# Kernel tuning notes

Measured on AMD Instinct MI355X. Metric: run time of the kernel, lower is better.

The kernel has to match this reference:

```python
import jax, jax.numpy as jnp
import numpy as np

LN2 = 0.6931471805599453

def ssp(x):
    # 'shifted_sp' activation: softplus(x) - log(2)
    return jax.nn.softplus(x) - LN2

def _res_chain(x, W1, b1, W2, b2):
    # PhysNetResidual chain: x <- lin2(ssp(lin1(ssp(x)))) + x
    # W1/W2: [n_res, F, F], b1/b2: [n_res, F]
    for j in range(W1.shape[0]):
        h = ssp(x) @ W1[j] + b1[j]
        x = ssp(h) @ W2[j] + b2[j] + x
    return x

def _physnet_module(feat, radial_aev, idx12, p):
    (W_I, b_I, W_J, b_J, W_gate, gvec, W_int, b_int,
     ri_W1, ri_b1, ri_W2, ri_b2,
     ra_W1, ra_b1, ra_W2, ra_b2,
     ro_W1, ro_b1, ro_W2, ro_b2, W_out, b_out) = p
    N, F = feat.shape
    # self term (no species are dummy -> non_dummy indexing is identity)
    h_self = ssp(ssp(feat) @ W_I + b_I)                       # [N,F]
    # pair messages
    gate = radial_aev @ W_gate                                 # [P,F] (no bias)
    f12 = feat[idx12]                                          # [2,P,F] gather
    fm = ssp(ssp(f12) @ W_J + b_J)                             # [2,P,F]
    pair_msg = gate[None] * fm                                 # [2,P,F]
    proto = jnp.zeros_like(feat).at[idx12.reshape(-1)].add(
        pair_msg.reshape(-1, F))                               # scatter-add
    proto = proto + h_self
    msg = _res_chain(proto, ri_W1, ri_b1, ri_W2, ri_b2)
    feat2 = feat * gvec + ssp(msg) @ W_int + b_int
    feat2 = _res_chain(feat2, ra_W1, ra_b1, ra_W2, ra_b2)
    e = ssp(_res_chain(feat2, ro_W1, ro_b1, ro_W2, ro_b2)) @ W_out + b_out  # [N]
    return e, feat2

def setup_inputs() -> dict:
    key = jax.random.key(0)
    L, F, R = 5, 128, 64
    M, A = 128, 64
    N = M * A
    P = 400000
    ks = jax.random.split(key, 20)
    s = 0.05  # small weight scale keeps activations stable across 5 modules
    inp = {
        'species': jax.random.randint(ks[0], (M, A), 0, 4, dtype=jnp.int32),
        'features': jax.random.normal(ks[1], (N, F), jnp.float32),
        'radial_aev': jax.random.uniform(ks[2], (P, R), jnp.float32),
        'atom_index12': jax.random.randint(ks[3], (2, P), 0, N, dtype=jnp.int32),
        'W_I': jax.random.normal(ks[4], (L, F, F)) * s,
        'b_I': jnp.zeros((L, F)),
        'W_J': jax.random.normal(ks[5], (L, F, F)) * s,
        'b_J': jnp.zeros((L, F)),
        'W_gate': jax.random.normal(ks[6], (L, R, F)) * s,
        'gvec': jnp.ones((L, F)),
        'W_int': jax.random.normal(ks[7], (L, F, F)) * s,
        'b_int': jnp.zeros((L, F)),
        'ri_W1': jax.random.normal(ks[8], (L, 3, F, F)) * s,
        'ri_b1': jnp.zeros((L, 3, F)),
        'ri_W2': jax.random.normal(ks[9], (L, 3, F, F)) * s,
        'ri_b2': jnp.zeros((L, 3, F)),
        'ra_W1': jax.random.normal(ks[10], (L, 2, F, F)) * s,
        'ra_b1': jnp.zeros((L, 2, F)),
        'ra_W2': jax.random.normal(ks[11], (L, 2, F, F)) * s,
        'ra_b2': jnp.zeros((L, 2, F)),
        'ro_W1': jax.random.normal(ks[12], (L, 1, F, F)) * s,
        'ro_b1': jnp.zeros((L, 1, F)),
        'ro_W2': jax.random.normal(ks[13], (L, 1, F, F)) * s,
        'ro_b2': jnp.zeros((L, 1, F)),
        'W_out': jax.random.normal(ks[14], (L, F)) * s,
        'b_out': jnp.zeros((L,)),
    }
    return inp

def reference(species, features, radial_aev, atom_index12,
              W_I, b_I, W_J, b_J, W_gate, gvec, W_int, b_int,
              ri_W1, ri_b1, ri_W2, ri_b2,
              ra_W1, ra_b1, ra_W2, ra_b2,
              ro_W1, ro_b1, ro_W2, ro_b2, W_out, b_out):
    M, A = species.shape
    params = (W_I, b_I, W_J, b_J, W_gate, gvec, W_int, b_int,
              ri_W1, ri_b1, ri_W2, ri_b2,
              ra_W1, ra_b1, ra_W2, ra_b2,
              ro_W1, ro_b1, ro_W2, ro_b2, W_out, b_out)
    feat = features
    energies = jnp.zeros((M * A,), features.dtype)
    for l in range(W_I.shape[0]):  # fixed small module loop
        p = tuple(arr[l] for arr in params)
        e, feat = _physnet_module(feat, radial_aev, atom_index12, p)
        energies = energies + e
    return energies.reshape(M, A), feat
```

## Files before the change

### kernel.cpp

```cpp
#include <hip/hip_runtime.h>


#define LN2F 0.69314718055994530942f
#define NB 128

using short8  = __attribute__((ext_vector_type(8))) short;
using float4v = __attribute__((ext_vector_type(4))) float;
typedef const __attribute__((address_space(1))) unsigned int* gas1_t;
typedef __attribute__((address_space(3))) unsigned int* las3_t;

__device__ __forceinline__ float sspf(float x) {
  float ax = fabsf(x);
  return fmaxf(x, 0.0f) + __logf(1.0f + __expf(-ax)) - LN2F;
}

__device__ __forceinline__ unsigned short f2bf(float x) {
  return (unsigned short)((__float_as_uint(x) + 0x8000u) >> 16);
}

__device__ __forceinline__ unsigned short f2bf_ne(float x) {
  unsigned int u = __float_as_uint(x);
  u += 0x7fffu + ((u >> 16) & 1u);
  return (unsigned short)(u >> 16);
}

__device__ __forceinline__ void dma16(const void* g, void* l) {
  __builtin_amdgcn_global_load_lds((gas1_t)(unsigned long long)g,
                                   (las3_t)(unsigned long long)l, 16, 0, 0);
}

__device__ __forceinline__ void dma32k(const unsigned short* g, unsigned short* l,
                                       int w, int lane) {
  const char* gb = (const char*)g + w * 2048 + lane * 16;
  char* lb = (char*)l + w * 2048;
  dma16(gb, lb);
  dma16(gb + 1024, lb + 1024);
}
__device__ __forceinline__ void dma16k(const unsigned short* g, unsigned short* l,
                                       int w, int lane) {
  dma16((const char*)g + w * 1024 + lane * 16, (char*)l + w * 1024);
}

__global__ __launch_bounds__(256) void hist_pass(const int* __restrict__ idx,
                                                 unsigned int* __restrict__ H,
                                                 int n2p, int C) {
  __shared__ unsigned int h[8192];
  int b = blockIdx.x, tid = threadIdx.x;
  for (int i = tid; i < 8192; i += 256) h[i] = 0;
  __syncthreads();
  int s = b * C, e = min(s + C, n2p);
  for (int i = s + tid; i < e; i += 256) atomicAdd(&h[idx[i]], 1u);
  __syncthreads();
  for (int i = tid; i < 8192; i += 256) H[(size_t)b * 8192 + i] = h[i];
}

__global__ __launch_bounds__(256) void col_scan(unsigned int* __restrict__ H,
                                                unsigned int* __restrict__ tot) {
  int a = blockIdx.x * 256 + threadIdx.x;
  unsigned int run = 0;
  for (int b = 0; b < NB; ++b) {
    unsigned int v = H[(size_t)b * 8192 + a];
    H[(size_t)b * 8192 + a] = run;
    run += v;
  }
  tot[a] = run;
}

__global__ __launch_bounds__(256) void scan_kernel(const unsigned int* __restrict__ cnt,
                                                   unsigned int* __restrict__ off, int NA) {
  int t = threadIdx.x;
  unsigned int local[32], s = 0;
#pragma unroll
  for (int i = 0; i < 32; ++i) { local[i] = cnt[t * 32 + i]; s += local[i]; }
  unsigned int v = s;
  int lane = t & 63, w = t >> 6;
#pragma unroll
  for (int o = 1; o < 64; o <<= 1) {
    unsigned int u = __shfl_up(v, o, 64);
    if (lane >= o) v += u;
  }
  __shared__ unsigned int wt4[4];
  if (lane == 63) wt4[w] = v;
  __syncthreads();
  unsigned int base = 0;
  for (int k = 0; k < w; ++k) base += wt4[k];
  unsigned int excl = base + v - s;
#pragma unroll
  for (int i = 0; i < 32; ++i) { off[t * 32 + i] = excl; excl += local[i]; }
  if (t == 255) off[NA] = excl;
}

__global__ __launch_bounds__(256) void place_pass(const int* __restrict__ idx,
                                                  const unsigned int* __restrict__ H,
                                                  const unsigned int* __restrict__ off,
                                                  unsigned int* __restrict__ pairid,
                                                  int P, int C) {
  __shared__ unsigned int pos[8192];
  int b = blockIdx.x, tid = threadIdx.x;
  for (int i = tid; i < 8192; i += 256)
    pos[i] = off[i] + H[(size_t)b * 8192 + i];
  __syncthreads();
  int n2p = 2 * P;
  int s = b * C, e = min(s + C, n2p);
  for (int i = s + tid; i < e; i += 256) {
    int a = idx[i];
    unsigned int p = atomicAdd(&pos[a], 1u);
    pairid[p] = (i >= P) ? (unsigned int)(i - P) : (unsigned int)i;
  }
}

__global__ __launch_bounds__(256) void gather_kernel(const float* __restrict__ radial,
                                                     const unsigned int* __restrict__ off,
                                                     const unsigned int* __restrict__ pairid,
                                                     float* __restrict__ S) {
  __shared__ float red[3][64];
  int a = blockIdx.x;
  int lane = threadIdx.x & 63, w = threadIdx.x >> 6;
  unsigned int b = off[a], e = off[a + 1];
  float acc = 0.0f;
  for (unsigned int base = b + w; base < e; base += 32) {
    unsigned int pp[8];
    float vv[8];
#pragma unroll
    for (int k = 0; k < 8; ++k) {
      unsigned int j = base + 4 * k;
      pp[k] = pairid[j < e ? j : b];
    }
#pragma unroll
    for (int k = 0; k < 8; ++k) vv[k] = radial[(size_t)pp[k] * 64 + lane];
#pragma unroll
    for (int k = 0; k < 8; ++k) {
      unsigned int j = base + 4 * k;
      acc += (j < e) ? vv[k] : 0.0f;
    }
  }
  if (w > 0) red[w - 1][lane] = acc;
  __syncthreads();
  if (w == 0) {
    acc += red[0][lane] + red[1][lane] + red[2][lane];
    S[(size_t)a * 64 + lane] = acc;
  }
}

struct PrepArgs {
  const float* src[80];
  int isgate[80];
};

__global__ __launch_bounds__(256) void prep_weights(PrepArgs A, unsigned short* __restrict__ Wt) {
  int m = blockIdx.x;
  const float* s = A.src[m];
  unsigned short* d = Wt + (size_t)m * 16384;
  if (!A.isgate[m]) {
    for (int it = 0; it < 8; ++it) {
      int q = threadIdx.x + it * 256;
      int n = q & 127, j = q >> 7;
      unsigned short tmp[8];
#pragma unroll
      for (int cc = 0; cc < 8; ++cc) tmp[cc] = f2bf_ne(s[(8 * j + cc) * 128 + n]);
      *(uint4*)(d + (n * 16 + (j ^ (n & 15))) * 8) = *(uint4*)tmp;
    }
  } else {
    for (int it = 0; it < 4; ++it) {
      int q = threadIdx.x + it * 256;
      int n = q & 127, j = q >> 7;
      unsigned short tmp[8];
#pragma unroll
      for (int cc = 0; cc < 8; ++cc) tmp[cc] = f2bf_ne(s[(8 * j + cc) * 128 + n]);
      *(uint4*)(d + (n * 8 + (j ^ (n & 7))) * 8) = *(uint4*)tmp;
    }
  }
}

struct BiasArgs {
  const float* p[17];
  int stride[17];
  const float* b_out;
};

__global__ __launch_bounds__(256) void pack_bias(BiasArgs B, float* __restrict__ dst) {
  int l = blockIdx.x;
  for (int i = threadIdx.x; i < 17 * 128; i += 256) {
    int s = i >> 7;
    dst[(size_t)l * 2304 + i] = B.p[s][l * B.stride[s] + (i & 127)];
  }
  if (threadIdx.x == 0) dst[(size_t)l * 2304 + 17 * 128] = B.b_out[l];
}

struct ChainArgs {
  const float* feat_in;
  const float* S;
  const unsigned short* wt;
  const float* bias_pack;
  float* feat_out;
  float* energy;
};

__device__ __forceinline__ void gemm128s(const unsigned short* sA_, const unsigned short* sW,
                                         int arow, int col0, int l16, int quad, float4v* acc) {
  const unsigned short* ar = sA_ + (arow + l16) * 136 + quad * 8;
  short8 a0 = *(const short8*)(ar);
  short8 a1 = *(const short8*)(ar + 32);
  short8 a2 = *(const short8*)(ar + 64);
  short8 a3 = *(const short8*)(ar + 96);
  const unsigned short* bb = sW + col0 * 128;
  *acc = __builtin_amdgcn_mfma_f32_16x16x32_bf16(a0, *(const short8*)(bb + ((quad + 0) ^ l16) * 8), *acc, 0, 0, 0);
  *acc = __builtin_amdgcn_mfma_f32_16x16x32_bf16(a1, *(const short8*)(bb + ((quad + 4) ^ l16) * 8), *acc, 0, 0, 0);
  *acc = __builtin_amdgcn_mfma_f32_16x16x32_bf16(a2, *(const short8*)(bb + ((quad + 8) ^ l16) * 8), *acc, 0, 0, 0);
  *acc = __builtin_amdgcn_mfma_f32_16x16x32_bf16(a3, *(const short8*)(bb + ((quad + 12) ^ l16) * 8), *acc, 0, 0, 0);
}

__device__ __forceinline__ void gemm64s(const unsigned short* sS_, const unsigned short* sW,
                                        int arow, int col0, int l16, int quad, float4v* acc) {
  const unsigned short* ar = sS_ + (arow + l16) * 72 + quad * 8;
  short8 a0 = *(const short8*)(ar);
  short8 a1 = *(const short8*)(ar + 32);
  int l8 = l16 & 7;
  const unsigned short* bb = sW + col0 * 64;
  *acc = __builtin_amdgcn_mfma_f32_16x16x32_bf16(a0, *(const short8*)(bb + ((quad + 0) ^ l8) * 8), *acc, 0, 0, 0);
  *acc = __builtin_amdgcn_mfma_f32_16x16x32_bf16(a1, *(const short8*)(bb + ((quad + 4) ^ l8) * 8), *acc, 0, 0, 0);
}

__device__ __forceinline__ void write_ssp_A(unsigned short* sA_, const float4v v,
                                            int arow, int col0, int quad) {
#pragma unroll
  for (int r = 0; r < 4; ++r)
    sA_[(arow + quad * 4 + r) * 136 + col0] = f2bf(sspf(v[r]));
}

__global__ __launch_bounds__(1024, 4) void chain_kernel(ChainArgs A) {
  __shared__ __align__(16) unsigned short swb[2][16384];
  __shared__ __align__(16) unsigned short sA[2][32 * 136];
  __shared__ __align__(16) unsigned short sS[32 * 72];
  __shared__ float sBias[2304];
  __shared__ float sE[32];

  const int tid  = threadIdx.x;
  const int row0 = blockIdx.x * 32;
  const int lane = tid & 63;
  const int w    = tid >> 6;
  const int g    = w >> 3;
  const int c    = w & 7;
  const int l16  = lane & 15;
  const int quad = lane >> 4;
  const int arow = 16 * g;
  const int col0 = 16 * c + l16;

  dma16k(A.wt, swb[0], w, lane);

  for (int i = tid; i < 32 * 64; i += 1024) {
    int r = i >> 6, k = i & 63;
    sS[r * 72 + k] = f2bf(A.S[(size_t)(row0 + r) * 64 + k]);
  }
  for (int i = tid; i < 32 * 128; i += 1024) {
    int r = i >> 7, k = i & 127;
    sA[0][r * 136 + k] = f2bf(sspf(A.feat_in[(size_t)(row0 + r) * 128 + k]));
  }
  float4v ff;
#pragma unroll
  for (int r = 0; r < 4; ++r)
    ff[r] = A.feat_in[(size_t)(row0 + arow + quad * 4 + r) * 128 + col0];
  if (tid < 32) sE[tid] = 0.0f;
  __syncthreads();

  const float4v Z = {0.f, 0.f, 0.f, 0.f};
  float4v gG, fm, xf, t4;
  float p0 = 0.f, p1 = 0.f, p2 = 0.f, p3 = 0.f, bsum = 0.f;

#pragma unroll 1
  for (int l = 0; l < 5; ++l) {
    const size_t slot0 = (size_t)l * 16 * 16384;

    dma32k(A.wt + slot0 + 16384, swb[1], w, lane);
    for (int i = tid; i < 2304; i += 1024) sBias[i] = A.bias_pack[(size_t)l * 2304 + i];
    gG = Z;
    gemm64s(sS, swb[0], arow, col0, l16, quad, &gG);
    __syncthreads();

    dma32k(A.wt + slot0 + 2 * 16384, swb[0], w, lane);
    fm = Z;
    gemm128s(sA[0], swb[1], arow, col0, l16, quad, &fm);
    {
      float bv = sBias[0 * 128 + col0];
#pragma unroll
      for (int r = 0; r < 4; ++r) fm[r] = sspf(fm[r] + bv);
    }
    __syncthreads();

    dma32k(A.wt + slot0 + 3 * 16384, swb[1], w, lane);
    t4 = Z;
    gemm128s(sA[0], swb[0], arow, col0, l16, quad, &t4);
    {
      float bv = sBias[1 * 128 + col0];
#pragma unroll
      for (int r = 0; r < 4; ++r) xf[r] = fm[r] * gG[r] + sspf(t4[r] + bv);
    }
    write_ssp_A(sA[1], xf, arow, col0, quad);
    __syncthreads();

#pragma unroll
    for (int jj = 0; jj < 3; ++jj) {
      const int th = 3 + 2 * jj;
      dma32k(A.wt + slot0 + (size_t)(th + 1) * 16384, swb[th & 1 ? 0 : 1], w, lane);
      t4 = Z;
      gemm128s(sA[1], swb[th & 1], arow, col0, l16, quad, &t4);
      {
        float bv = sBias[(th - 1) * 128 + col0];
#pragma unroll
        for (int r = 0; r < 4; ++r) t4[r] += bv;
      }
      write_ssp_A(sA[0], t4, arow, col0, quad);
      __syncthreads();

      const int tx = th + 1;
      dma32k(A.wt + slot0 + (size_t)(tx + 1) * 16384, swb[tx & 1 ? 0 : 1], w, lane);
      t4 = Z;
      gemm128s(sA[0], swb[tx & 1], arow, col0, l16, quad, &t4);
      {
        float bv = sBias[(tx - 1) * 128 + col0];
#pragma unroll
        for (int r = 0; r < 4; ++r) xf[r] += t4[r] + bv;
      }
      write_ssp_A(sA[1], xf, arow, col0, quad);
      __syncthreads();
    }

    dma32k(A.wt + slot0 + 10 * 16384, swb[0], w, lane);
    t4 = Z;
    gemm128s(sA[1], swb[1], arow, col0, l16, quad, &t4);
    {
      float bv = sBias[8 * 128 + col0];
      float gv = sBias[15 * 128 + col0];
#pragma unroll
      for (int r = 0; r < 4; ++r) xf[r] = ff[r] * gv + t4[r] + bv;
    }
    write_ssp_A(sA[0], xf, arow, col0, quad);
    __syncthreads();

#pragma unroll
    for (int jj = 0; jj < 2; ++jj) {
      const int th = 10 + 2 * jj;
      dma32k(A.wt + slot0 + (size_t)(th + 1) * 16384, swb[th & 1 ? 0 : 1], w, lane);
      t4 = Z;
      gemm128s(sA[0], swb[th & 1], arow, col0, l16, quad, &t4);
      {
        float bv = sBias[(th - 1) * 128 + col0];
#pragma unroll
        for (int r = 0; r < 4; ++r) t4[r] += bv;
      }
      write_ssp_A(sA[1], t4, arow, col0, quad);
      __syncthreads();

      const int tx = th + 1;
      dma32k(A.wt + slot0 + (size_t)(tx + 1) * 16384, swb[tx & 1 ? 0 : 1], w, lane);
      t4 = Z;
      gemm128s(sA[1], swb[tx & 1], arow, col0, l16, quad, &t4);
      {
        float bv = sBias[(tx - 1) * 128 + col0];
#pragma unroll
        for (int r = 0; r < 4; ++r) xf[r] += t4[r] + bv;
      }
      write_ssp_A(sA[0], xf, arow, col0, quad);
      __syncthreads();
    }

    ff = xf;
    if (l == 4) {
#pragma unroll
      for (int r = 0; r < 4; ++r)
        A.feat_out[(size_t)(row0 + arow + quad * 4 + r) * 128 + col0] = xf[r];
    }

    dma32k(A.wt + slot0 + 15 * 16384, swb[1], w, lane);
    t4 = Z;
    gemm128s(sA[0], swb[0], arow, col0, l16, quad, &t4);
    {
      float bv = sBias[13 * 128 + col0];
#pragma unroll
      for (int r = 0; r < 4; ++r) t4[r] += bv;
    }
    write_ssp_A(sA[1], t4, arow, col0, quad);
    __syncthreads();

    if (l < 4) dma16k(A.wt + slot0 + 16 * 16384, swb[0], w, lane);
    t4 = Z;
    gemm128s(sA[1], swb[1], arow, col0, l16, quad, &t4);
    {
      float bv = sBias[14 * 128 + col0];
      float wv = sBias[16 * 128 + col0];
      p0 += sspf(xf[0] + t4[0] + bv) * wv;
      p1 += sspf(xf[1] + t4[1] + bv) * wv;
      p2 += sspf(xf[2] + t4[2] + bv) * wv;
      p3 += sspf(xf[3] + t4[3] + bv) * wv;
    }
    bsum += sBias[17 * 128];
    __syncthreads();
  }

#pragma unroll
  for (int o = 1; o < 16; o <<= 1) {
    p0 += __shfl_xor(p0, o, 64);
    p1 += __shfl_xor(p1, o, 64);
    p2 += __shfl_xor(p2, o, 64);
    p3 += __shfl_xor(p3, o, 64);
  }
  if (l16 == 0) {
    atomicAdd(&sE[arow + quad * 4 + 0], p0);
    atomicAdd(&sE[arow + quad * 4 + 1], p1);
    atomicAdd(&sE[arow + quad * 4 + 2], p2);
    atomicAdd(&sE[arow + quad * 4 + 3], p3);
  }
  __syncthreads();
  if (tid < 32) A.energy[row0 + tid] = sE[tid] + bsum;
}

extern "C" void kernel_launch(void* const* d_in, const int* in_sizes, int n_in,
                              void* d_out, int out_size, void* d_ws, size_t ws_size,
                              hipStream_t stream) {
  const float* features = (const float*)d_in[1];
  const float* radial   = (const float*)d_in[2];
  const int*   idx12    = (const int*)  d_in[3];
  const float* W_I    = (const float*)d_in[4];
  const float* b_I    = (const float*)d_in[5];
  const float* W_J    = (const float*)d_in[6];
  const float* b_J    = (const float*)d_in[7];
  const float* W_gate = (const float*)d_in[8];
  const float* gvec   = (const float*)d_in[9];
  const float* W_int  = (const float*)d_in[10];
  const float* b_int  = (const float*)d_in[11];
  const float* ri_W1  = (const float*)d_in[12];
  const float* ri_b1  = (const float*)d_in[13];
  const float* ri_W2  = (const float*)d_in[14];
  const float* ri_b2  = (const float*)d_in[15];
  const float* ra_W1  = (const float*)d_in[16];
  const float* ra_b1  = (const float*)d_in[17];
  const float* ra_W2  = (const float*)d_in[18];
  const float* ra_b2  = (const float*)d_in[19];
  const float* ro_W1  = (const float*)d_in[20];
  const float* ro_b1  = (const float*)d_in[21];
  const float* ro_W2  = (const float*)d_in[22];
  const float* ro_b2  = (const float*)d_in[23];
  const float* W_out  = (const float*)d_in[24];
  const float* b_out  = (const float*)d_in[25];

  const int N = in_sizes[1] / 128;
  const int P = in_sizes[3] / 2;
  const int L = in_sizes[25];
  const int n2p = 2 * P;
  const int C = (n2p + NB - 1) / NB;

  float* S = (float*)d_ws;
  float* bias_pack = S + (size_t)N * 64;
  unsigned short* Wt = (unsigned short*)(bias_pack + 5 * 2304);
  unsigned int* H      = (unsigned int*)(Wt + (size_t)80 * 16384);
  unsigned int* tot    = H + (size_t)NB * 8192;
  unsigned int* off    = tot + N;
  unsigned int* pairid = off + N + 4;

  PrepArgs pa;
  for (int l = 0; l < L; ++l) {
    const float* fx[16] = {
      W_gate + l * 8192,
      W_J + l * 16384, W_I + l * 16384,
      ri_W1 + (l * 3 + 0) * 16384, ri_W2 + (l * 3 + 0) * 16384,
      ri_W1 + (l * 3 + 1) * 16384, ri_W2 + (l * 3 + 1) * 16384,
      ri_W1 + (l * 3 + 2) * 16384, ri_W2 + (l * 3 + 2) * 16384,
      W_int + l * 16384,
      ra_W1 + (l * 2 + 0) * 16384, ra_W2 + (l * 2 + 0) * 16384,
      ra_W1 + (l * 2 + 1) * 16384, ra_W2 + (l * 2 + 1) * 16384,
      ro_W1 + l * 16384, ro_W2 + l * 16384 };
    for (int t = 0; t < 16; ++t) { pa.src[l * 16 + t] = fx[t]; pa.isgate[l * 16 + t] = (t == 0); }
  }
  prep_weights<<<80, 256, 0, stream>>>(pa, Wt);

  BiasArgs ba;
  const float* bp[17] = { b_J, b_I,
    ri_b1, ri_b2, ri_b1 + 128, ri_b2 + 128, ri_b1 + 256, ri_b2 + 256,
    b_int, ra_b1, ra_b2, ra_b1 + 128, ra_b2 + 128, ro_b1, ro_b2, gvec, W_out };
  int st[17] = {128,128, 384,384,384,384,384,384, 128, 256,256,256,256, 128,128,128,128};
  for (int q = 0; q < 17; ++q) { ba.p[q] = bp[q]; ba.stride[q] = st[q]; }
  ba.b_out = b_out;
  pack_bias<<<5, 256, 0, stream>>>(ba, bias_pack);

  hist_pass<<<NB, 256, 0, stream>>>(idx12, H, n2p, C);
  col_scan<<<32, 256, 0, stream>>>(H, tot);
  scan_kernel<<<1, 256, 0, stream>>>(tot, off, N);
  place_pass<<<NB, 256, 0, stream>>>(idx12, H, off, pairid, P, C);
  gather_kernel<<<N, 256, 0, stream>>>(radial, off, pairid, S);

  ChainArgs ca;
  ca.feat_in   = features;
  ca.S         = S;
  ca.wt        = Wt;
  ca.bias_pack = bias_pack;
  ca.energy    = (float*)d_out;
  ca.feat_out  = (float*)d_out + N;
  chain_kernel<<<N / 32, 1024, 0, stream>>>(ca);
}
```

Before: 347.3 us.

## Merge prep kernels, fold scan into place pass, vectorize gather, restructure chain pipeline

Combines weight prep, bias packing and histogram into one launch, and folds the global scan into each place_pass block so the single-block scan launch disappears. The gather now loads float4 rows, with 16 lanes per pair, and reduces with shuffles. The chain kernel keeps the gate weight in its own LDS buffer, double-buffers the bias pack and prefetches the next module's weights and bias. It also precomputes per-lane LDS pointers through macros. The aim is fewer kernel launches, less serialization between module iterations, and cheaper address arithmetic, paid for with more LDS per block and redundant scan work in every place_pass block.

```diff
diff --git a/kernel.cpp b/kernel.cpp
--- a/kernel.cpp
+++ b/kernel.cpp
@@ -41,17 +41,60 @@
   dma16((const char*)g + w * 1024 + lane * 16, (char*)l + w * 1024);
 }
 
-__global__ __launch_bounds__(256) void hist_pass(const int* __restrict__ idx,
-                                                 unsigned int* __restrict__ H,
-                                                 int n2p, int C) {
+struct K1Args {
+  const float* wsrc[80];
+  int isgate[80];
+  const float* bp[17];
+  int bstride[17];
+  const float* b_out;
+  const int* idx;
+  unsigned short* Wt;
+  float* bias_pack;
+  unsigned int* H;
+  int n2p, C;
+};
+
+__global__ __launch_bounds__(256) void k1_prep(K1Args K) {
   __shared__ unsigned int h[8192];
   int b = blockIdx.x, tid = threadIdx.x;
-  for (int i = tid; i < 8192; i += 256) h[i] = 0;
-  __syncthreads();
-  int s = b * C, e = min(s + C, n2p);
-  for (int i = s + tid; i < e; i += 256) atomicAdd(&h[idx[i]], 1u);
-  __syncthreads();
-  for (int i = tid; i < 8192; i += 256) H[(size_t)b * 8192 + i] = h[i];
+  if (b < 80) {
+    const float* s = K.wsrc[b];
+    unsigned short* d = K.Wt + (size_t)b * 16384;
+    if (!K.isgate[b]) {
+      for (int it = 0; it < 8; ++it) {
+        int q = tid + it * 256;
+        int n = q & 127, j = q >> 7;
+        unsigned short tmp[8];
+#pragma unroll
+        for (int cc = 0; cc < 8; ++cc) tmp[cc] = f2bf_ne(s[(8 * j + cc) * 128 + n]);
+        *(uint4*)(d + (n * 16 + (j ^ (n & 15))) * 8) = *(uint4*)tmp;
+      }
+    } else {
+      for (int it = 0; it < 4; ++it) {
+        int q = tid + it * 256;
+        int n = q & 127, j = q >> 7;
+        unsigned short tmp[8];
+#pragma unroll
+        for (int cc = 0; cc < 8; ++cc) tmp[cc] = f2bf_ne(s[(8 * j + cc) * 128 + n]);
+        *(uint4*)(d + (n * 8 + (j ^ (n & 7))) * 8) = *(uint4*)tmp;
+      }
+    }
+  } else if (b < 85) {
+    int l = b - 80;
+    for (int i = tid; i < 17 * 128; i += 256) {
+      int s = i >> 7;
+      K.bias_pack[(size_t)l * 2304 + i] = K.bp[s][l * K.bstride[s] + (i & 127)];
+    }
+    if (tid == 0) K.bias_pack[(size_t)l * 2304 + 17 * 128] = K.b_out[l];
+  } else {
+    int blk = b - 85;
+    for (int i = tid; i < 8192; i += 256) h[i] = 0;
+    __syncthreads();
+    int s = blk * K.C, e = min(s + K.C, K.n2p);
+    for (int i = s + tid; i < e; i += 256) atomicAdd(&h[K.idx[i]], 1u);
+    __syncthreads();
+    for (int i = tid; i < 8192; i += 256) K.H[(size_t)blk * 8192 + i] = h[i];
+  }
 }
 
 __global__ __launch_bounds__(256) void col_scan(unsigned int* __restrict__ H,
@@ -66,43 +109,43 @@
   tot[a] = run;
 }
 
-__global__ __launch_bounds__(256) void scan_kernel(const unsigned int* __restrict__ cnt,
-                                                   unsigned int* __restrict__ off, int NA) {
-  int t = threadIdx.x;
+__global__ __launch_bounds__(256) void place_pass(const int* __restrict__ idx,
+                                                  const unsigned int* __restrict__ H,
+                                                  const unsigned int* __restrict__ tot,
+                                                  unsigned int* __restrict__ off_out,
+                                                  unsigned int* __restrict__ pairid,
+                                                  int P, int C) {
+  __shared__ unsigned int pos[8192];
+  __shared__ unsigned int wt4[4];
+  int b = blockIdx.x, tid = threadIdx.x;
   unsigned int local[32], s = 0;
 #pragma unroll
-  for (int i = 0; i < 32; ++i) { local[i] = cnt[t * 32 + i]; s += local[i]; }
+  for (int i = 0; i < 32; ++i) { local[i] = tot[tid * 32 + i]; s += local[i]; }
   unsigned int v = s;
-  int lane = t & 63, w = t >> 6;
+  int lane = tid & 63, wv = tid >> 6;
 #pragma unroll
   for (int o = 1; o < 64; o <<= 1) {
     unsigned int u = __shfl_up(v, o, 64);
     if (lane >= o) v += u;
   }
-  __shared__ unsigned int wt4[4];
-  if (lane == 63) wt4[w] = v;
+  if (lane == 63) wt4[wv] = v;
   __syncthreads();
   unsigned int base = 0;
-  for (int k = 0; k < w; ++k) base += wt4[k];
+  for (int k = 0; k < wv; ++k) base += wt4[k];
   unsigned int excl = base + v - s;
 #pragma unroll
-  for (int i = 0; i < 32; ++i) { off[t * 32 + i] = excl; excl += local[i]; }
-  if (t == 255) off[NA] = excl;
-}
-
-__global__ __launch_bounds__(256) void place_pass(const int* __restrict__ idx,
-                                                  const unsigned int* __restrict__ H,
-                                                  const unsigned int* __restrict__ off,
-                                                  unsigned int* __restrict__ pairid,
-                                                  int P, int C) {
-  __shared__ unsigned int pos[8192];
-  int b = blockIdx.x, tid = threadIdx.x;
-  for (int i = tid; i < 8192; i += 256)
-    pos[i] = off[i] + H[(size_t)b * 8192 + i];
+  for (int i = 0; i < 32; ++i) {
+    pos[tid * 32 + i] = excl;
+    if (b == 0) off_out[tid * 32 + i] = excl;
+    excl += local[i];
+  }
+  if (b == 0 && tid == 255) off_out[8192] = excl;
+  __syncthreads();
+  for (int i = tid; i < 8192; i += 256) pos[i] += H[(size_t)b * 8192 + i];
   __syncthreads();
   int n2p = 2 * P;
-  int s = b * C, e = min(s + C, n2p);
-  for (int i = s + tid; i < e; i += 256) {
+  int s2 = b * C, e2 = min(s2 + C, n2p);
+  for (int i = s2 + tid; i < e2; i += 256) {
     int a = idx[i];
     unsigned int p = atomicAdd(&pos[a], 1u);
     pairid[p] = (i >= P) ? (unsigned int)(i - P) : (unsigned int)i;
@@ -113,78 +156,42 @@
                                                      const unsigned int* __restrict__ off,
                                                      const unsigned int* __restrict__ pairid,
                                                      float* __restrict__ S) {
-  __shared__ float red[3][64];
+  __shared__ float4v red[3][16];
   int a = blockIdx.x;
   int lane = threadIdx.x & 63, w = threadIdx.x >> 6;
+  int grp = lane >> 4, l16v = lane & 15;
   unsigned int b = off[a], e = off[a + 1];
-  float acc = 0.0f;
-  for (unsigned int base = b + w; base < e; base += 32) {
+  float4v acc = {0.f, 0.f, 0.f, 0.f};
+  for (unsigned int base = b; base < e; base += 128) {
     unsigned int pp[8];
-    float vv[8];
 #pragma unroll
     for (int k = 0; k < 8; ++k) {
-      unsigned int j = base + 4 * k;
+      unsigned int j = base + k * 16 + w * 4 + grp;
       pp[k] = pairid[j < e ? j : b];
     }
-#pragma unroll
-    for (int k = 0; k < 8; ++k) vv[k] = radial[(size_t)pp[k] * 64 + lane];
+    float4v vv[8];
+#pragma unroll
+    for (int k = 0; k < 8; ++k)
+      vv[k] = *(const float4v*)(radial + (size_t)pp[k] * 64 + l16v * 4);
 #pragma unroll
     for (int k = 0; k < 8; ++k) {
-      unsigned int j = base + 4 * k;
-      acc += (j < e) ? vv[k] : 0.0f;
+      unsigned int j = base + k * 16 + w * 4 + grp;
+      if (j < e) acc += vv[k];
     }
   }
-  if (w > 0) red[w - 1][lane] = acc;
-  __syncthreads();
-  if (w == 0) {
-    acc += red[0][lane] + red[1][lane] + red[2][lane];
-    S[(size_t)a * 64 + lane] = acc;
-  }
-}
-
-struct PrepArgs {
-  const float* src[80];
-  int isgate[80];
-};
-
-__global__ __launch_bounds__(256) void prep_weights(PrepArgs A, unsigned short* __restrict__ Wt) {
-  int m = blockIdx.x;
-  const float* s = A.src[m];
-  unsigned short* d = Wt + (size_t)m * 16384;
-  if (!A.isgate[m]) {
-    for (int it = 0; it < 8; ++it) {
-      int q = threadIdx.x + it * 256;
-      int n = q & 127, j = q >> 7;
-      unsigned short tmp[8];
-#pragma unroll
-      for (int cc = 0; cc < 8; ++cc) tmp[cc] = f2bf_ne(s[(8 * j + cc) * 128 + n]);
-      *(uint4*)(d + (n * 16 + (j ^ (n & 15))) * 8) = *(uint4*)tmp;
-    }
-  } else {
-    for (int it = 0; it < 4; ++it) {
-      int q = threadIdx.x + it * 256;
-      int n = q & 127, j = q >> 7;
-      unsigned short tmp[8];
-#pragma unroll
-      for (int cc = 0; cc < 8; ++cc) tmp[cc] = f2bf_ne(s[(8 * j + cc) * 128 + n]);
-      *(uint4*)(d + (n * 8 + (j ^ (n & 7))) * 8) = *(uint4*)tmp;
-    }
-  }
-}
-
-struct BiasArgs {
-  const float* p[17];
-  int stride[17];
-  const float* b_out;
-};
-
-__global__ __launch_bounds__(256) void pack_bias(BiasArgs B, float* __restrict__ dst) {
-  int l = blockIdx.x;
-  for (int i = threadIdx.x; i < 17 * 128; i += 256) {
-    int s = i >> 7;
-    dst[(size_t)l * 2304 + i] = B.p[s][l * B.stride[s] + (i & 127)];
-  }
-  if (threadIdx.x == 0) dst[(size_t)l * 2304 + 17 * 128] = B.b_out[l];
+#pragma unroll
+  for (int o = 16; o < 64; o <<= 1) {
+#pragma unroll
+    for (int cc = 0; cc < 4; ++cc) acc[cc] += __shfl_xor(acc[cc], o, 64);
+  }
+  if (w > 0 && grp == 0) red[w - 1][l16v] = acc;
+  __syncthreads();
+  if (w == 0 && grp == 0) {
+    acc += red[0][l16v];
+    acc += red[1][l16v];
+    acc += red[2][l16v];
+    *(float4v*)(S + (size_t)a * 64 + l16v * 4) = acc;
+  }
 }
 
 struct ChainArgs {
@@ -196,43 +203,122 @@
   float* energy;
 };
 
-__device__ __forceinline__ void gemm128s(const unsigned short* sA_, const unsigned short* sW,
-                                         int arow, int col0, int l16, int quad, float4v* acc) {
-  const unsigned short* ar = sA_ + (arow + l16) * 136 + quad * 8;
-  short8 a0 = *(const short8*)(ar);
-  short8 a1 = *(const short8*)(ar + 32);
-  short8 a2 = *(const short8*)(ar + 64);
-  short8 a3 = *(const short8*)(ar + 96);
-  const unsigned short* bb = sW + col0 * 128;
-  *acc = __builtin_amdgcn_mfma_f32_16x16x32_bf16(a0, *(const short8*)(bb + ((quad + 0) ^ l16) * 8), *acc, 0, 0, 0);
-  *acc = __builtin_amdgcn_mfma_f32_16x16x32_bf16(a1, *(const short8*)(bb + ((quad + 4) ^ l16) * 8), *acc, 0, 0, 0);
-  *acc = __builtin_amdgcn_mfma_f32_16x16x32_bf16(a2, *(const short8*)(bb + ((quad + 8) ^ l16) * 8), *acc, 0, 0, 0);
-  *acc = __builtin_amdgcn_mfma_f32_16x16x32_bf16(a3, *(const short8*)(bb + ((quad + 12) ^ l16) * 8), *acc, 0, 0, 0);
-}
-
-__device__ __forceinline__ void gemm64s(const unsigned short* sS_, const unsigned short* sW,
-                                        int arow, int col0, int l16, int quad, float4v* acc) {
-  const unsigned short* ar = sS_ + (arow + l16) * 72 + quad * 8;
-  short8 a0 = *(const short8*)(ar);
-  short8 a1 = *(const short8*)(ar + 32);
-  int l8 = l16 & 7;
-  const unsigned short* bb = sW + col0 * 64;
-  *acc = __builtin_amdgcn_mfma_f32_16x16x32_bf16(a0, *(const short8*)(bb + ((quad + 0) ^ l8) * 8), *acc, 0, 0, 0);
-  *acc = __builtin_amdgcn_mfma_f32_16x16x32_bf16(a1, *(const short8*)(bb + ((quad + 4) ^ l8) * 8), *acc, 0, 0, 0);
-}
-
-__device__ __forceinline__ void write_ssp_A(unsigned short* sA_, const float4v v,
-                                            int arow, int col0, int quad) {
-#pragma unroll
-  for (int r = 0; r < 4; ++r)
-    sA_[(arow + quad * 4 + r) * 136 + col0] = f2bf(sspf(v[r]));
-}
+#define MFMA_ __builtin_amdgcn_mfma_f32_16x16x32_bf16
+
+#define G128(AP, SP, ACC) { \
+  short8 a0_ = *(const short8*)(aB + (AP)*4352); \
+  short8 a1_ = *(const short8*)(aB + (AP)*4352 + 32); \
+  short8 a2_ = *(const short8*)(aB + (AP)*4352 + 64); \
+  short8 a3_ = *(const short8*)(aB + (AP)*4352 + 96); \
+  ACC = MFMA_(a0_, *(const short8*)(b0 + (SP)*16384), ACC, 0, 0, 0); \
+  ACC = MFMA_(a1_, *(const short8*)(b1 + (SP)*16384), ACC, 0, 0, 0); \
+  ACC = MFMA_(a2_, *(const short8*)(b2 + (SP)*16384), ACC, 0, 0, 0); \
+  ACC = MFMA_(a3_, *(const short8*)(b3 + (SP)*16384), ACC, 0, 0, 0); }
+
+#define WSSPM(AP, V) { \
+  wB[(AP)*4352]       = f2bf(sspf((V)[0])); \
+  wB[(AP)*4352 + 136] = f2bf(sspf((V)[1])); \
+  wB[(AP)*4352 + 272] = f2bf(sspf((V)[2])); \
+  wB[(AP)*4352 + 408] = f2bf(sspf((V)[3])); }
+
+#define MODBODY(S0) { \
+  const float* bl = &sB[(S0)][0]; \
+   \
+  dma32k(wtp + 2*16384, swb[(S0)^1], w, lane); \
+  gG = Z; \
+  { short8 s0_ = *(const short8*)(aS); short8 s1_ = *(const short8*)(aS + 32); \
+    gG = MFMA_(s0_, *(const short8*)(g0), gG, 0, 0, 0); \
+    gG = MFMA_(s1_, *(const short8*)(g1), gG, 0, 0, 0); } \
+  fm = Z; G128(0, (S0), fm); \
+  { float bv = bl[col0]; \
+    for (int r = 0; r < 4; ++r) fm[r] = sspf(fm[r] + bv); } \
+  __syncthreads(); \
+   \
+  dma32k(wtp + 3*16384, swb[(S0)], w, lane); \
+  if (l < 4) dma16k(wtp + 16*16384, sG, w, lane); \
+  t4 = Z; G128(0, (S0)^1, t4); \
+  { float bv = bl[128 + col0]; \
+    for (int r = 0; r < 4; ++r) xf[r] = fm[r]*gG[r] + sspf(t4[r] + bv); } \
+  WSSPM(1, xf); \
+  __syncthreads(); \
+   \
+  dma32k(wtp + 4*16384, swb[(S0)^1], w, lane); \
+  t4 = Z; G128(1, (S0), t4); \
+  { float bv = bl[2*128 + col0]; for (int r = 0; r < 4; ++r) t4[r] += bv; } \
+  WSSPM(0, t4); __syncthreads(); \
+  dma32k(wtp + 5*16384, swb[(S0)], w, lane); \
+  t4 = Z; G128(0, (S0)^1, t4); \
+  { float bv = bl[3*128 + col0]; for (int r = 0; r < 4; ++r) xf[r] += t4[r] + bv; } \
+  WSSPM(1, xf); __syncthreads(); \
+  dma32k(wtp + 6*16384, swb[(S0)^1], w, lane); \
+  t4 = Z; G128(1, (S0), t4); \
+  { float bv = bl[4*128 + col0]; for (int r = 0; r < 4; ++r) t4[r] += bv; } \
+  WSSPM(0, t4); __syncthreads(); \
+  dma32k(wtp + 7*16384, swb[(S0)], w, lane); \
+  t4 = Z; G128(0, (S0)^1, t4); \
+  { float bv = bl[5*128 + col0]; for (int r = 0; r < 4; ++r) xf[r] += t4[r] + bv; } \
+  WSSPM(1, xf); __syncthreads(); \
+  dma32k(wtp + 8*16384, swb[(S0)^1], w, lane); \
+  t4 = Z; G128(1, (S0), t4); \
+  { float bv = bl[6*128 + col0]; for (int r = 0; r < 4; ++r) t4[r] += bv; } \
+  WSSPM(0, t4); __syncthreads(); \
+  dma32k(wtp + 9*16384, swb[(S0)], w, lane); \
+  t4 = Z; G128(0, (S0)^1, t4); \
+  { float bv = bl[7*128 + col0]; for (int r = 0; r < 4; ++r) xf[r] += t4[r] + bv; } \
+  WSSPM(1, xf); __syncthreads(); \
+   \
+  dma32k(wtp + 10*16384, swb[(S0)^1], w, lane); \
+  t4 = Z; G128(1, (S0), t4); \
+  { float bv = bl[8*128 + col0]; float gv = bl[15*128 + col0]; \
+    for (int r = 0; r < 4; ++r) xf[r] = ff[r]*gv + t4[r] + bv; } \
+  WSSPM(0, xf); __syncthreads(); \
+   \
+  dma32k(wtp + 11*16384, swb[(S0)], w, lane); \
+  t4 = Z; G128(0, (S0)^1, t4); \
+  { float bv = bl[9*128 + col0]; for (int r = 0; r < 4; ++r) t4[r] += bv; } \
+  WSSPM(1, t4); __syncthreads(); \
+  dma32k(wtp + 12*16384, swb[(S0)^1], w, lane); \
+  t4 = Z; G128(1, (S0), t4); \
+  { float bv = bl[10*128 + col0]; for (int r = 0; r < 4; ++r) xf[r] += t4[r] + bv; } \
+  WSSPM(0, xf); __syncthreads(); \
+  dma32k(wtp + 13*16384, swb[(S0)], w, lane); \
+  t4 = Z; G128(0, (S0)^1, t4); \
+  { float bv = bl[11*128 + col0]; for (int r = 0; r < 4; ++r) t4[r] += bv; } \
+  WSSPM(1, t4); __syncthreads(); \
+  dma32k(wtp + 14*16384, swb[(S0)^1], w, lane); \
+  if (l < 4 && w < 9) \
+    dma16((const char*)A.bias_pack + (size_t)(l + 1) * 9216 + w * 1024 + lane * 16, \
+          (char*)&sB[(S0)^1][0] + w * 1024); \
+  t4 = Z; G128(1, (S0), t4); \
+  { float bv = bl[12*128 + col0]; for (int r = 0; r < 4; ++r) xf[r] += t4[r] + bv; } \
+  WSSPM(0, xf); __syncthreads(); \
+  ff = xf; \
+  if (l == 4) { \
+    for (int r = 0; r < 4; ++r) \
+      A.feat_out[(size_t)(row0 + arow + quad*4 + r) * 128 + col0] = xf[r]; \
+  } \
+   \
+  dma32k(wtp + 15*16384, swb[(S0)], w, lane); \
+  t4 = Z; G128(0, (S0)^1, t4); \
+  { float bv = bl[13*128 + col0]; for (int r = 0; r < 4; ++r) t4[r] += bv; } \
+  WSSPM(1, t4); __syncthreads(); \
+   \
+  if (l < 4) dma32k(wtp + 17*16384, swb[(S0)^1], w, lane); \
+  t4 = Z; G128(1, (S0), t4); \
+  { float bv = bl[14*128 + col0]; float wv = bl[16*128 + col0]; \
+    p0 += sspf(xf[0] + t4[0] + bv) * wv; \
+    p1 += sspf(xf[1] + t4[1] + bv) * wv; \
+    p2 += sspf(xf[2] + t4[2] + bv) * wv; \
+    p3 += sspf(xf[3] + t4[3] + bv) * wv; } \
+  bsum += bl[17*128]; \
+  __syncthreads(); }
 
 __global__ __launch_bounds__(1024, 4) void chain_kernel(ChainArgs A) {
   __shared__ __align__(16) unsigned short swb[2][16384];
+  __shared__ __align__(16) unsigned short sG[8192];
   __shared__ __align__(16) unsigned short sA[2][32 * 136];
   __shared__ __align__(16) unsigned short sS[32 * 72];
-  __shared__ float sBias[2304];
+  __shared__ __align__(16) float sB[2][2304];
   __shared__ float sE[32];
 
   const int tid  = threadIdx.x;
@@ -245,8 +331,22 @@
   const int quad = lane >> 4;
   const int arow = 16 * g;
   const int col0 = 16 * c + l16;
-
-  dma16k(A.wt, swb[0], w, lane);
+  const int l8   = l16 & 7;
+
+  const unsigned short* aB = &sA[0][0] + (arow + l16) * 136 + quad * 8;
+  unsigned short*       wB = &sA[0][0] + (arow + quad * 4) * 136 + col0;
+  const unsigned short* b0 = &swb[0][0] + col0 * 128 + (((quad + 0) ^ l16) * 8);
+  const unsigned short* b1 = &swb[0][0] + col0 * 128 + (((quad + 4) ^ l16) * 8);
+  const unsigned short* b2 = &swb[0][0] + col0 * 128 + (((quad + 8) ^ l16) * 8);
+  const unsigned short* b3 = &swb[0][0] + col0 * 128 + (((quad + 12) ^ l16) * 8);
+  const unsigned short* aS = &sS[0] + (arow + l16) * 72 + quad * 8;
+  const unsigned short* g0 = &sG[0] + col0 * 64 + (((quad + 0) ^ l8) * 8);
+  const unsigned short* g1 = &sG[0] + col0 * 64 + (((quad + 4) ^ l8) * 8);
+
+  dma16k(A.wt, sG, w, lane);
+  dma32k(A.wt + 16384, swb[0], w, lane);
+  if (w < 9)
+    dma16((const char*)A.bias_pack + w * 1024 + lane * 16, (char*)&sB[0][0] + w * 1024);
 
   for (int i = tid; i < 32 * 64; i += 1024) {
     int r = i >> 6, k = i & 63;
@@ -269,132 +369,8 @@
 
 #pragma unroll 1
   for (int l = 0; l < 5; ++l) {
-    const size_t slot0 = (size_t)l * 16 * 16384;
-
-    dma32k(A.wt + slot0 + 16384, swb[1], w, lane);
-    for (int i = tid; i < 2304; i += 1024) sBias[i] = A.bias_pack[(size_t)l * 2304 + i];
-    gG = Z;
-    gemm64s(sS, swb[0], arow, col0, l16, quad, &gG);
-    __syncthreads();
-
-    dma32k(A.wt + slot0 + 2 * 16384, swb[0], w, lane);
-    fm = Z;
-    gemm128s(sA[0], swb[1], arow, col0, l16, quad, &fm);
-    {
-      float bv = sBias[0 * 128 + col0];
-#pragma unroll
-      for (int r = 0; r < 4; ++r) fm[r] = sspf(fm[r] + bv);
-    }
-    __syncthreads();
-
-    dma32k(A.wt + slot0 + 3 * 16384, swb[1], w, lane);
-    t4 = Z;
-    gemm128s(sA[0], swb[0], arow, col0, l16, quad, &t4);
-    {
-      float bv = sBias[1 * 128 + col0];
-#pragma unroll
-      for (int r = 0; r < 4; ++r) xf[r] = fm[r] * gG[r] + sspf(t4[r] + bv);
-    }
-    write_ssp_A(sA[1], xf, arow, col0, quad);
-    __syncthreads();
-
-#pragma unroll
-    for (int jj = 0; jj < 3; ++jj) {
-      const int th = 3 + 2 * jj;
-      dma32k(A.wt + slot0 + (size_t)(th + 1) * 16384, swb[th & 1 ? 0 : 1], w, lane);
-      t4 = Z;
-      gemm128s(sA[1], swb[th & 1], arow, col0, l16, quad, &t4);
-      {
-        float bv = sBias[(th - 1) * 128 + col0];
-#pragma unroll
-        for (int r = 0; r < 4; ++r) t4[r] += bv;
-      }
-      write_ssp_A(sA[0], t4, arow, col0, quad);
-      __syncthreads();
-
-      const int tx = th + 1;
-      dma32k(A.wt + slot0 + (size_t)(tx + 1) * 16384, swb[tx & 1 ? 0 : 1], w, lane);
-      t4 = Z;
-      gemm128s(sA[0], swb[tx & 1], arow, col0, l16, quad, &t4);
-      {
-        float bv = sBias[(tx - 1) * 128 + col0];
-#pragma unroll
-        for (int r = 0; r < 4; ++r) xf[r] += t4[r] + bv;
-      }
-      write_ssp_A(sA[1], xf, arow, col0, quad);
-      __syncthreads();
-    }
-
-    dma32k(A.wt + slot0 + 10 * 16384, swb[0], w, lane);
-    t4 = Z;
-    gemm128s(sA[1], swb[1], arow, col0, l16, quad, &t4);
-    {
-      float bv = sBias[8 * 128 + col0];
-      float gv = sBias[15 * 128 + col0];
-#pragma unroll
-      for (int r = 0; r < 4; ++r) xf[r] = ff[r] * gv + t4[r] + bv;
-    }
-    write_ssp_A(sA[0], xf, arow, col0, quad);
-    __syncthreads();
-
-#pragma unroll
-    for (int jj = 0; jj < 2; ++jj) {
-      const int th = 10 + 2 * jj;
-      dma32k(A.wt + slot0 + (size_t)(th + 1) * 16384, swb[th & 1 ? 0 : 1], w, lane);
-      t4 = Z;
-      gemm128s(sA[0], swb[th & 1], arow, col0, l16, quad, &t4);
-      {
-        float bv = sBias[(th - 1) * 128 + col0];
-#pragma unroll
-        for (int r = 0; r < 4; ++r) t4[r] += bv;
-      }
-      write_ssp_A(sA[1], t4, arow, col0, quad);
-      __syncthreads();
-
-      const int tx = th + 1;
-      dma32k(A.wt + slot0 + (size_t)(tx + 1) * 16384, swb[tx & 1 ? 0 : 1], w, lane);
-      t4 = Z;
-      gemm128s(sA[1], swb[tx & 1], arow, col0, l16, quad, &t4);
-      {
-        float bv = sBias[(tx - 1) * 128 + col0];
-#pragma unroll
-        for (int r = 0; r < 4; ++r) xf[r] += t4[r] + bv;
-      }
-      write_ssp_A(sA[0], xf, arow, col0, quad);
-      __syncthreads();
-    }
-
-    ff = xf;
-    if (l == 4) {
-#pragma unroll
-      for (int r = 0; r < 4; ++r)
-        A.feat_out[(size_t)(row0 + arow + quad * 4 + r) * 128 + col0] = xf[r];
-    }
-
-    dma32k(A.wt + slot0 + 15 * 16384, swb[1], w, lane);
-    t4 = Z;
-    gemm128s(sA[0], swb[0], arow, col0, l16, quad, &t4);
-    {
-      float bv = sBias[13 * 128 + col0];
-#pragma unroll
-      for (int r = 0; r < 4; ++r) t4[r] += bv;
-    }
-    write_ssp_A(sA[1], t4, arow, col0, quad);
-    __syncthreads();
-
-    if (l < 4) dma16k(A.wt + slot0 + 16 * 16384, swb[0], w, lane);
-    t4 = Z;
-    gemm128s(sA[1], swb[1], arow, col0, l16, quad, &t4);
-    {
-      float bv = sBias[14 * 128 + col0];
-      float wv = sBias[16 * 128 + col0];
-      p0 += sspf(xf[0] + t4[0] + bv) * wv;
-      p1 += sspf(xf[1] + t4[1] + bv) * wv;
-      p2 += sspf(xf[2] + t4[2] + bv) * wv;
-      p3 += sspf(xf[3] + t4[3] + bv) * wv;
-    }
-    bsum += sBias[17 * 128];
-    __syncthreads();
+    const unsigned short* wtp = A.wt + (size_t)l * 16 * 16384;
+    if ((l & 1) == 0) MODBODY(0) else MODBODY(1)
   }
 
 #pragma unroll
@@ -457,7 +433,7 @@
   unsigned int* off    = tot + N;
   unsigned int* pairid = off + N + 4;
 
-  PrepArgs pa;
+  K1Args k1;
   for (int l = 0; l < L; ++l) {
     const float* fx[16] = {
       W_gate + l * 8192,
@@ -469,23 +445,20 @@
       ra_W1 + (l * 2 + 0) * 16384, ra_W2 + (l * 2 + 0) * 16384,
       ra_W1 + (l * 2 + 1) * 16384, ra_W2 + (l * 2 + 1) * 16384,
       ro_W1 + l * 16384, ro_W2 + l * 16384 };
-    for (int t = 0; t < 16; ++t) { pa.src[l * 16 + t] = fx[t]; pa.isgate[l * 16 + t] = (t == 0); }
-  }
-  prep_weights<<<80, 256, 0, stream>>>(pa, Wt);
-
-  BiasArgs ba;
+    for (int t = 0; t < 16; ++t) { k1.wsrc[l * 16 + t] = fx[t]; k1.isgate[l * 16 + t] = (t == 0); }
+  }
   const float* bp[17] = { b_J, b_I,
     ri_b1, ri_b2, ri_b1 + 128, ri_b2 + 128, ri_b1 + 256, ri_b2 + 256,
     b_int, ra_b1, ra_b2, ra_b1 + 128, ra_b2 + 128, ro_b1, ro_b2, gvec, W_out };
   int st[17] = {128,128, 384,384,384,384,384,384, 128, 256,256,256,256, 128,128,128,128};
-  for (int q = 0; q < 17; ++q) { ba.p[q] = bp[q]; ba.stride[q] = st[q]; }
-  ba.b_out = b_out;
-  pack_bias<<<5, 256, 0, stream>>>(ba, bias_pack);
-
-  hist_pass<<<NB, 256, 0, stream>>>(idx12, H, n2p, C);
+  for (int q = 0; q < 17; ++q) { k1.bp[q] = bp[q]; k1.bstride[q] = st[q]; }
+  k1.b_out = b_out;
+  k1.idx = idx12; k1.Wt = Wt; k1.bias_pack = bias_pack; k1.H = H;
+  k1.n2p = n2p; k1.C = C;
+  k1_prep<<<80 + 5 + NB, 256, 0, stream>>>(k1);
+
   col_scan<<<32, 256, 0, stream>>>(H, tot);
-  scan_kernel<<<1, 256, 0, stream>>>(tot, off, N);
-  place_pass<<<NB, 256, 0, stream>>>(idx12, H, off, pairid, P, C);
+  place_pass<<<NB, 256, 0, stream>>>(idx12, H, tot, off, pairid, P, C);
   gather_kernel<<<N, 256, 0, stream>>>(radial, off, pairid, S);
 
   ChainArgs ca;
```

Result: faster. 328.8 us (-5.3%).
